# Kernel tuning notes

Measured on AMD Instinct MI355X. Metric: run time of the kernel, lower is better.

## Reference

```python
import math
import jax, jax.numpy as jnp
import numpy as np

DIM = 1536; NH = 12; HD = DIM // NH        # head_dim = 128
F, H, W = 4, 20, 26
S = F * H * W                              # 2080 tokens
BLOCK = 128
SPAD = math.ceil(S / BLOCK) * BLOCK        # 2176
EPS = 1e-6
C = HD // 2
SF, SH, SW = C - 2 * (C // 3), C // 3, C // 3   # 22, 21, 21 rotary bands


def _rope_params(max_len, d, theta=10000.0):
    inv = 1.0 / (theta ** (np.arange(0, d, 2, dtype=np.float64) / d))
    return np.outer(np.arange(max_len), inv)   # [max_len, d//2] angles


def _rope(x, freqs, f, h, w):
    # x: [b, s, n, d] with s == f*h*w; freqs: [1024, d//2] angles
    b, s, n, d = x.shape
    ang = jnp.concatenate([
        jnp.broadcast_to(freqs[:f, :SF][:, None, None, :], (f, h, w, SF)),
        jnp.broadcast_to(freqs[:h, SF:SF + SH][None, :, None, :], (f, h, w, SH)),
        jnp.broadcast_to(freqs[:w, SF + SH:C][None, None, :, :], (f, h, w, SW)),
    ], axis=-1).reshape(s, C)
    cos = jnp.cos(ang)[None, :, None, :]
    sin = jnp.sin(ang)[None, :, None, :]
    xr = x.reshape(b, s, n, C, 2)
    x0, x1 = xr[..., 0], xr[..., 1]          # complex mult (x0+ix1)*(cos+isin)
    out = jnp.stack([x0 * cos - x1 * sin, x0 * sin + x1 * cos], axis=-1)
    return out.reshape(b, s, n, d)


def setup_inputs():
    key = jax.random.key(0)
    ks = jax.random.split(key, 6)
    freqs = jnp.asarray(np.concatenate([
        _rope_params(1024, 2 * SF), _rope_params(1024, 2 * SH), _rope_params(1024, 2 * SW)
    ], axis=1), dtype=jnp.float32)           # [1024, 64]
    lin = lambda k: jax.random.normal(k, (DIM, DIM), jnp.float32) * 0.02
    blk = jnp.arange(SPAD) // BLOCK
    # block-causal (128-token blocks) mask, padding keys (>= S) masked out
    mask = (blk[:, None] >= blk[None, :]) & (jnp.arange(SPAD)[None, :] < S)
    return {
        "x": jax.random.normal(ks[0], (1, S, DIM), jnp.float32),
        "freqs": freqs,
        "wq": lin(ks[1]), "bq": jnp.zeros((DIM,), jnp.float32),
        "wk": lin(ks[2]), "bk": jnp.zeros((DIM,), jnp.float32),
        "wv": lin(ks[3]), "bv": jnp.zeros((DIM,), jnp.float32),
        "wo": lin(ks[4]), "bo": jnp.zeros((DIM,), jnp.float32),
        "gq": jnp.ones((DIM,), jnp.float32),
        "gk": jnp.ones((DIM,), jnp.float32),
        "seq_lens": jnp.array([S], jnp.int32),
        "grid_sizes": jnp.array([[F, H, W]], jnp.int32),
        "mask": mask,
    }


def reference(x, freqs, wq, bq, wk, bk, wv, bv, wo, bo, gq, gk, seq_lens, grid_sizes, mask):
    b, s, _ = x.shape
    n, d = NH, HD
    rms = lambda t, g: (t * jax.lax.rsqrt(jnp.mean(t * t, axis=-1, keepdims=True) + EPS)) * g
    q = rms(x @ wq + bq, gq).reshape(b, s, n, d)
    k = rms(x @ wk + bk, gk).reshape(b, s, n, d)
    v = (x @ wv + bv).reshape(b, s, n, d)
    f, h, w = int(grid_sizes[0, 0]), int(grid_sizes[0, 1]), int(grid_sizes[0, 2])
    sl = int(seq_lens[0])
    if sl > 0 and s == 2 * sl:  # teacher forcing: rope each half independently
        q = jnp.concatenate([_rope(q[:, :sl], freqs, f, h, w), _rope(q[:, sl:], freqs, f, h, w)], axis=1)
        k = jnp.concatenate([_rope(k[:, :sl], freqs, f, h, w), _rope(k[:, sl:], freqs, f, h, w)], axis=1)
    else:
        q = _rope(q, freqs, f, h, w)
        k = _rope(k, freqs, f, h, w)
    pad = SPAD - s
    if pad > 0:
        pz = ((0, 0), (0, pad), (0, 0), (0, 0))
        q, k, v = jnp.pad(q, pz), jnp.pad(k, pz), jnp.pad(v, pz)
    scores = jnp.einsum('bqnd,bknd->bnqk', q, k) / math.sqrt(d)
    scores = jnp.where(mask[None, None], scores, -jnp.inf)
    attn = jax.nn.softmax(scores, axis=-1)
    o = jnp.einsum('bnqk,bknd->bqnd', attn, v)[:, :s].reshape(b, s, n * d)
    return o @ wo + bo
```

## Files before the change

### kernel.cpp

```cpp
#include <hip/hip_runtime.h>

#define DIMM   1536
#define NHEAD  12
#define HD     128
#define SEQ    2080
#define SPADN  2176
#define HWPROD 520
#define SCALE  0.08838834764831845f
#define K2F    0.12751744154f

typedef short short8  __attribute__((ext_vector_type(8)));
typedef float floatx4 __attribute__((ext_vector_type(4)));

__device__ __forceinline__ unsigned short f2bf(float f) {
    union { float f; unsigned u; } v; v.f = f;
    return (unsigned short)((v.u + 0x7fffu + ((v.u >> 16) & 1u)) >> 16);
}
__device__ __forceinline__ float bf2f(unsigned short u) {
    union { unsigned u; float f; } v; v.u = ((unsigned)u) << 16;
    return v.f;
}

__device__ __forceinline__ void gld_lds16(const void* g, void* l) {
    __builtin_amdgcn_global_load_lds(
        (const __attribute__((address_space(1))) unsigned int*)g,
        (__attribute__((address_space(3))) unsigned int*)l, 16, 0, 0);
}

__constant__ int c_base4[34] = {0,1,2,3, 4,6,8,10, 12,15,18,21, 24,28,32,36,
                                40,45,50,55, 60,66,72,78, 84,91,98,105,
                                112,120,128,136, 144, 153};
#define SLOTS_PER_HEAD 153

__global__ void k_prep(const float* __restrict__ x,
                       const float* __restrict__ w0, const float* __restrict__ w1,
                       const float* __restrict__ w2, const float* __restrict__ w3,
                       unsigned short* __restrict__ xb,
                       unsigned short* __restrict__ t0, unsigned short* __restrict__ t1,
                       unsigned short* __restrict__ t2, unsigned short* __restrict__ t3) {
    int z = blockIdx.z;
    if (z == 4) {
        int n4 = SEQ * DIMM / 4;
        int idx = (blockIdx.y * 24 + blockIdx.x) * 256 + threadIdx.x;
#pragma unroll
        for (int i = 0; i < 6; i++) {
            int p = idx + i * 147456;
            if (p < n4) {
                float4 v = ((const float4*)x)[p];
                ushort4 o;
                o.x = f2bf(v.x); o.y = f2bf(v.y); o.z = f2bf(v.z); o.w = f2bf(v.w);
                ((ushort4*)xb)[p] = o;
            }
        }
        return;
    }
    const float* in = (z == 0) ? w0 : (z == 1) ? w1 : (z == 2) ? w2 : w3;
    unsigned short* out = (z == 0) ? t0 : (z == 1) ? t1 : (z == 2) ? t2 : t3;
    __shared__ float tile[64][65];
    int tx = threadIdx.x & 63, ty = threadIdx.x >> 6;
    int r0 = blockIdx.x * 64, c0 = blockIdx.y * 64;
#pragma unroll
    for (int i = 0; i < 16; i++)
        tile[i * 4 + ty][tx] = in[(size_t)(r0 + i * 4 + ty) * DIMM + c0 + tx];
    __syncthreads();
#pragma unroll
    for (int i = 0; i < 16; i++) {
        int cc = i * 4 + ty;
        out[(size_t)(c0 + cc) * DIMM + r0 + tx] = f2bf(tile[tx][cc]);
    }
}

__global__ __launch_bounds__(256, 3) void k_gemm(
    const unsigned short* __restrict__ A,
    const unsigned short* __restrict__ B0, const unsigned short* __restrict__ B1,
    const unsigned short* __restrict__ B2,
    const float* __restrict__ bias0, const float* __restrict__ bias1, const float* __restrict__ bias2,
    unsigned short* __restrict__ Qh, unsigned short* __restrict__ Kh,
    unsigned short* __restrict__ Vt,
    int M, int N, int K) {
    const unsigned short* B = B0; const float* bias = bias0;
    if (blockIdx.z == 1) { B = B1; bias = bias1; }
    if (blockIdx.z == 2) { B = B2; bias = bias2; }

    __shared__ unsigned short As[128 * 64];
    __shared__ unsigned short Bs[128 * 64];

    int tid = threadIdx.x;
    int lane = tid & 63, wv = tid >> 6;
    int quad = lane >> 4, l16 = lane & 15;
    int m0 = blockIdx.y * 128, n0 = blockIdx.x * 128;
    int wm = (wv >> 1) * 64, wn = (wv & 1) * 64;
    int sw = l16 & 7;

    int srow_in_blk = lane >> 3;
    int schunk = lane & 7;
    int gchunk = schunk ^ (srow_in_blk & 7);

    floatx4 acc[4][4];
#pragma unroll
    for (int i = 0; i < 4; i++)
#pragma unroll
        for (int j = 0; j < 4; j++) acc[i][j] = (floatx4){0.f, 0.f, 0.f, 0.f};

    for (int k0 = 0; k0 < K; k0 += 64) {
#pragma unroll
        for (int i = 0; i < 4; i++) {
            int blkrow = (wv * 4 + i) * 8;
            int r = blkrow + srow_in_blk;
            int ra = m0 + r; if (ra > M - 1) ra = M - 1;
            gld_lds16(A + (size_t)ra * K + k0 + gchunk * 8, &As[blkrow * 64]);
            gld_lds16(B + (size_t)(n0 + r) * K + k0 + gchunk * 8, &Bs[blkrow * 64]);
        }
        __syncthreads();
#pragma unroll
        for (int kc = 0; kc < 2; kc++) {
            short8 af[4], bfr[4];
#pragma unroll
            for (int t = 0; t < 4; t++) {
                int ca = ((kc * 4 + quad) ^ sw) << 3;
                af[t]  = *(const short8*)&As[(wm + t * 16 + l16) * 64 + ca];
                bfr[t] = *(const short8*)&Bs[(wn + t * 16 + l16) * 64 + ca];
            }
#pragma unroll
            for (int mi = 0; mi < 4; mi++)
#pragma unroll
                for (int ni = 0; ni < 4; ni++)
                    acc[mi][ni] = __builtin_amdgcn_mfma_f32_16x16x32_bf16(af[mi], bfr[ni], acc[mi][ni], 0, 0, 0);
        }
        __syncthreads();
    }
    if (blockIdx.z == 2) {
#pragma unroll
        for (int mi = 0; mi < 4; mi++) {
            int row0 = m0 + wm + mi * 16 + quad * 4;
            if (row0 < M) {
#pragma unroll
                for (int ni = 0; ni < 4; ni++) {
                    int col = n0 + wn + ni * 16 + l16;
                    float b = bias[col];
                    ushort4 o;
                    o.x = f2bf(acc[mi][ni][0] + b);
                    o.y = f2bf(acc[mi][ni][1] + b);
                    o.z = f2bf(acc[mi][ni][2] + b);
                    o.w = f2bf(acc[mi][ni][3] + b);
                    *(ushort4*)(Vt + (size_t)col * SPADN + row0) = o;
                }
            }
        }
    } else {
        unsigned short* O = (blockIdx.z == 0) ? Qh : Kh;
#pragma unroll
        for (int mi = 0; mi < 4; mi++) {
#pragma unroll
            for (int r = 0; r < 4; r++) {
                int row = m0 + wm + mi * 16 + quad * 4 + r;
                if (row < M) {
#pragma unroll
                    for (int ni = 0; ni < 4; ni++) {
                        int col = n0 + wn + ni * 16 + l16;
                        O[(size_t)row * DIMM + col] = f2bf(acc[mi][ni][r] + bias[col]);
                    }
                }
            }
        }
    }
}

__global__ __launch_bounds__(256, 8) void k_gemm64(
    const unsigned short* __restrict__ A, const unsigned short* __restrict__ B,
    const float* __restrict__ bias, float* __restrict__ C, int M, int N, int K) {
    __shared__ unsigned short As[64 * 64];
    __shared__ unsigned short Bs[64 * 64];
    int tid = threadIdx.x;
    int lane = tid & 63, wv = tid >> 6;
    int quad = lane >> 4, l16 = lane & 15;
    int m0 = blockIdx.y * 64, n0 = blockIdx.x * 64;
    int wm = (wv >> 1) * 32, wn = (wv & 1) * 32;

    int srow = lane >> 3;
    int schunk = lane & 7;

    floatx4 acc[2][2];
#pragma unroll
    for (int i = 0; i < 2; i++)
#pragma unroll
        for (int j = 0; j < 2; j++) acc[i][j] = (floatx4){0.f, 0.f, 0.f, 0.f};

    for (int k0 = 0; k0 < K; k0 += 64) {
#pragma unroll
        for (int i = 0; i < 2; i++) {
            int rb = (i * 4 + wv) * 8;
            int r = rb + srow;
            int g = schunk ^ (r & 7);
            int ra = m0 + r; if (ra > M - 1) ra = M - 1;
            gld_lds16(A + (size_t)ra * K + k0 + g * 8, &As[rb * 64]);
            gld_lds16(B + (size_t)(n0 + r) * K + k0 + g * 8, &Bs[rb * 64]);
        }
        __syncthreads();
#pragma unroll
        for (int kc = 0; kc < 2; kc++) {
            short8 af[2], bfr[2];
#pragma unroll
            for (int t = 0; t < 2; t++) {
                int rowa = wm + t * 16 + l16;
                int rowb = wn + t * 16 + l16;
                int c = kc * 4 + quad;
                af[t]  = *(const short8*)&As[rowa * 64 + ((c ^ (rowa & 7)) << 3)];
                bfr[t] = *(const short8*)&Bs[rowb * 64 + ((c ^ (rowb & 7)) << 3)];
            }
#pragma unroll
            for (int mi = 0; mi < 2; mi++)
#pragma unroll
                for (int ni = 0; ni < 2; ni++)
                    acc[mi][ni] = __builtin_amdgcn_mfma_f32_16x16x32_bf16(af[mi], bfr[ni], acc[mi][ni], 0, 0, 0);
        }
        __syncthreads();
    }
#pragma unroll
    for (int mi = 0; mi < 2; mi++) {
#pragma unroll
        for (int r = 0; r < 4; r++) {
            int row = m0 + wm + mi * 16 + quad * 4 + r;
            if (row < M) {
#pragma unroll
                for (int ni = 0; ni < 2; ni++) {
                    int col = n0 + wn + ni * 16 + l16;
                    C[(size_t)row * N + col] = acc[mi][ni][r] + bias[col];
                }
            }
        }
    }
}

__global__ void k_rmsrope(const unsigned short* __restrict__ Qh, const unsigned short* __restrict__ Kh,
                          const float* __restrict__ gq, const float* __restrict__ gk,
                          const float* __restrict__ freqs,
                          unsigned short* __restrict__ Qa, unsigned short* __restrict__ Ka) {
    __shared__ float redq[4], redk[4];
    int s = blockIdx.x;
    int tid = threadIdx.x;
    int lane = tid & 63, wv = tid >> 6;
    const ushort2* qrow = (const ushort2*)(Qh + (size_t)s * DIMM);
    const ushort2* krow = (const ushort2*)(Kh + (size_t)s * DIMM);
    const float2* g2q = (const float2*)gq;
    const float2* g2k = (const float2*)gk;

    float2 qv[3], kv[3];
    float sq = 0.f, sk = 0.f;
#pragma unroll
    for (int j = 0; j < 3; j++) {
        int p = tid + j * 256;
        ushort2 uq = qrow[p], uk = krow[p];
        qv[j].x = bf2f(uq.x); qv[j].y = bf2f(uq.y);
        kv[j].x = bf2f(uk.x); kv[j].y = bf2f(uk.y);
        sq += qv[j].x * qv[j].x + qv[j].y * qv[j].y;
        sk += kv[j].x * kv[j].x + kv[j].y * kv[j].y;
    }
#pragma unroll
    for (int m = 32; m >= 1; m >>= 1) { sq += __shfl_xor(sq, m); sk += __shfl_xor(sk, m); }
    if (lane == 0) { redq[wv] = sq; redk[wv] = sk; }
    __syncthreads();
    float tq = redq[0] + redq[1] + redq[2] + redq[3];
    float tk = redk[0] + redk[1] + redk[2] + redk[3];
    float scq = rsqrtf(tq * (1.f / DIMM) + 1e-6f);
    float sck = rsqrtf(tk * (1.f / DIMM) + 1e-6f);

    int fi = s / HWPROD;
    int rem = s - fi * HWPROD;
    int hi = rem / 26;
    int wi = rem - hi * 26;
#pragma unroll
    for (int j = 0; j < 3; j++) {
        int p = tid + j * 256;
        int c = p & 63;
        int pos = (c < 22) ? fi : ((c < 43) ? hi : wi);
        float ang = freqs[pos * 64 + c];
        float sn, cs;
        __sincosf(ang, &sn, &cs);
        float2 gqa = g2q[p];
        float q0 = qv[j].x * scq * gqa.x, q1 = qv[j].y * scq * gqa.y;
        ushort2 oq; oq.x = f2bf(q0 * cs - q1 * sn); oq.y = f2bf(q0 * sn + q1 * cs);
        float2 gka = g2k[p];
        float kk0 = kv[j].x * sck * gka.x, kk1 = kv[j].y * sck * gka.y;
        ushort2 ok; ok.x = f2bf(kk0 * cs - kk1 * sn); ok.y = f2bf(kk0 * sn + kk1 * cs);
        int h = p >> 6;
        size_t off = ((size_t)h * SPADN + s) * HD + 2 * c;
        *(ushort2*)(Qa + off) = oq;
        *(ushort2*)(Ka + off) = ok;
    }
}

__global__ __launch_bounds__(256, 3) void k_attn1(const unsigned short* __restrict__ Qa,
                                                  const unsigned short* __restrict__ Ka,
                                                  const unsigned short* __restrict__ Vt,
                                                  unsigned short* __restrict__ Opart,
                                                  float* __restrict__ Lpart,
                                                  unsigned short* __restrict__ Ob) {
    int s = blockIdx.x, h = blockIdx.y;
    int j = 0;
    while (j < 32 && c_base4[j + 1] <= s) j++;
    int z = s - c_base4[j];
    int nkb = (j >> 1) * 2 + 2;
    if (nkb > 33) nkb = 33;
    int nc = (nkb + 3) >> 2;
    int kb0 = z * 4;
    int kb1 = kb0 + 4; if (kb1 > nkb) kb1 = nkb;

    __shared__ unsigned short Ks[64 * 128];
    __shared__ unsigned short Vs[128 * 64];
    __shared__ unsigned short Ps[4][16][72];

    int tid = threadIdx.x;
    int lane = tid & 63, wv = tid >> 6;
    int quad = lane >> 4, l16 = lane & 15;
    int qrow0 = j * 64 + wv * 16;

    short8 qf[4];
#pragma unroll
    for (int kc = 0; kc < 4; kc++)
        qf[kc] = *(const short8*)(Qa + ((size_t)h * SPADN + qrow0 + l16) * HD + kc * 32 + quad * 8);

    short8 ones8;
#pragma unroll
    for (int i = 0; i < 8; i++) ones8[i] = (short)0x3F80;

    floatx4 of[8], of9;
#pragma unroll
    for (int ni = 0; ni < 8; ni++) of[ni] = (floatx4){0.f, 0.f, 0.f, 0.f};
    of9 = (floatx4){0.f, 0.f, 0.f, 0.f};

    int krow = lane >> 4;
    int kslot = lane & 15;
    int vrow = lane >> 3;
    int vslot = lane & 7;

    for (int kb = kb0; kb < kb1; kb++) {
        const unsigned short* kbase = Ka + (((size_t)h * SPADN + kb * 64) * HD);
#pragma unroll
        for (int i = 0; i < 4; i++) {
            int rb = i * 4 + wv;
            int r = rb * 4 + krow;
            int g = (kslot & 8) | ((kslot & 7) ^ (r & 7));
            gld_lds16(kbase + r * 128 + g * 8, &Ks[rb * 512]);
        }
#pragma unroll
        for (int i = 0; i < 4; i++) {
            int rb = i * 4 + wv;
            int r = rb * 8 + vrow;
            int g = vslot ^ (r & 7);
            gld_lds16(Vt + ((size_t)h * HD + r) * SPADN + kb * 64 + g * 8, &Vs[rb * 512]);
        }
        __syncthreads();

        floatx4 sa[4];
#pragma unroll
        for (int ni = 0; ni < 4; ni++) sa[ni] = (floatx4){0.f, 0.f, 0.f, 0.f};
#pragma unroll
        for (int kc = 0; kc < 4; kc++) {
            int c = kc * 4 + quad;
            short8 kf[4];
#pragma unroll
            for (int ni = 0; ni < 4; ni++) {
                int row = ni * 16 + l16;
                int slot = (c & 8) | ((c & 7) ^ (row & 7));
                kf[ni] = *(const short8*)&Ks[row * 128 + slot * 8];
            }
#pragma unroll
            for (int ni = 0; ni < 4; ni++)
                sa[ni] = __builtin_amdgcn_mfma_f32_16x16x32_bf16(qf[kc], kf[ni], sa[ni], 0, 0, 0);
        }

        if (kb != 32) {
#pragma unroll
            for (int r = 0; r < 4; r++) {
#pragma unroll
                for (int ni = 0; ni < 4; ni++) {
                    float p = exp2f(sa[ni][r] * K2F);
                    Ps[wv][quad * 4 + r][ni * 16 + l16] =
                        (unsigned short)(__float_as_uint(p) >> 16);
                }
            }
        } else {
#pragma unroll
            for (int r = 0; r < 4; r++) {
#pragma unroll
                for (int ni = 0; ni < 4; ni++) {
                    bool pad = (kb * 64 + ni * 16 + l16 >= SEQ);
                    float p = pad ? 0.f : exp2f(sa[ni][r] * K2F);
                    Ps[wv][quad * 4 + r][ni * 16 + l16] =
                        (unsigned short)(__float_as_uint(p) >> 16);
                }
            }
        }
#pragma unroll
        for (int kc = 0; kc < 2; kc++) {
            int ko = kc * 32 + quad * 8;
            int c = kc * 4 + quad;
            short8 pf = *(const short8*)&Ps[wv][l16][ko];
#pragma unroll
            for (int ni = 0; ni < 8; ni++) {
                int row = ni * 16 + l16;
                short8 vf = *(const short8*)&Vs[row * 64 + ((c ^ (row & 7)) << 3)];
                of[ni] = __builtin_amdgcn_mfma_f32_16x16x32_bf16(pf, vf, of[ni], 0, 0, 0);
            }
            of9 = __builtin_amdgcn_mfma_f32_16x16x32_bf16(pf, ones8, of9, 0, 0, 0);
        }
        __syncthreads();
    }

    if (nc == 1) {
#pragma unroll
        for (int r = 0; r < 4; r++) {
            float inv = 1.f / of9[r];
            int row = qrow0 + quad * 4 + r;
#pragma unroll
            for (int ni = 0; ni < 8; ni++)
                Ob[(size_t)row * DIMM + h * HD + ni * 16 + l16] = f2bf(of[ni][r] * inv);
        }
    } else {
        int slot = h * SLOTS_PER_HEAD + s;
        unsigned short* Op = Opart + (size_t)slot * 8192;
#pragma unroll
        for (int r = 0; r < 4; r++) {
            int lrow = wv * 16 + quad * 4 + r;
#pragma unroll
            for (int ni = 0; ni < 8; ni++)
                Op[lrow * 128 + ni * 16 + l16] = f2bf(of[ni][r]);
        }
        if (l16 == 0) {
#pragma unroll
            for (int r = 0; r < 4; r++)
                Lpart[slot * 64 + wv * 16 + quad * 4 + r] = of9[r];
        }
    }
}

__global__ void k_attn2(const unsigned short* __restrict__ Opart,
                        const float* __restrict__ Lpart,
                        unsigned short* __restrict__ Ob) {
    int j = blockIdx.x, h = blockIdx.y;
    int nkb = (j >> 1) * 2 + 2; if (nkb > 33) nkb = 33;
    int nc = (nkb + 3) >> 2;
    if (nc == 1) return;
    int base = h * SLOTS_PER_HEAD + c_base4[j];
    int t = threadIdx.x;
    int r = t >> 2;
    int c0 = (t & 3) * 32;
    int row = j * 64 + r;
    if (row >= SEQ) return;

    float acc[32];
#pragma unroll
    for (int q = 0; q < 32; q++) acc[q] = 0.f;
    float L = 0.f;
    for (int c = 0; c < nc; c++) {
        int slot = base + c;
        L += Lpart[slot * 64 + r];
        const ushort4* op = (const ushort4*)(Opart + (size_t)slot * 8192 + r * 128 + c0);
#pragma unroll
        for (int q = 0; q < 8; q++) {
            ushort4 u = op[q];
            acc[q * 4 + 0] += bf2f(u.x); acc[q * 4 + 1] += bf2f(u.y);
            acc[q * 4 + 2] += bf2f(u.z); acc[q * 4 + 3] += bf2f(u.w);
        }
    }
    float inv = 1.f / L;
    unsigned short* ob = Ob + (size_t)row * DIMM + h * HD + c0;
#pragma unroll
    for (int q = 0; q < 8; q++) {
        ushort4 o;
        o.x = f2bf(acc[q * 4 + 0] * inv); o.y = f2bf(acc[q * 4 + 1] * inv);
        o.z = f2bf(acc[q * 4 + 2] * inv); o.w = f2bf(acc[q * 4 + 3] * inv);
        *(ushort4*)(ob + q * 4) = o;
    }
}

extern "C" void kernel_launch(void* const* d_in, const int* in_sizes, int n_in,
                              void* d_out, int out_size, void* d_ws, size_t ws_size,
                              hipStream_t stream) {
    const float* x     = (const float*)d_in[0];
    const float* freqs = (const float*)d_in[1];
    const float* wq    = (const float*)d_in[2];
    const float* bq    = (const float*)d_in[3];
    const float* wk    = (const float*)d_in[4];
    const float* bk    = (const float*)d_in[5];
    const float* wv    = (const float*)d_in[6];
    const float* bv    = (const float*)d_in[7];
    const float* wo    = (const float*)d_in[8];
    const float* bo    = (const float*)d_in[9];
    const float* gq    = (const float*)d_in[10];
    const float* gk    = (const float*)d_in[11];
    float* out = (float*)d_out;

    char* ws = (char*)d_ws;
    size_t off = 0;
    auto alloc = [&](size_t bytes) -> void* {
        void* p = ws + off;
        off += (bytes + 255) & ~(size_t)255;
        return p;
    };
    unsigned short* xb  = (unsigned short*)alloc((size_t)SPADN * DIMM * 2);
    unsigned short* wqT = (unsigned short*)alloc((size_t)DIMM * DIMM * 2);
    unsigned short* wkT = (unsigned short*)alloc((size_t)DIMM * DIMM * 2);
    unsigned short* wvT = (unsigned short*)alloc((size_t)DIMM * DIMM * 2);
    unsigned short* Qh  = (unsigned short*)alloc((size_t)SEQ * DIMM * 2);
    unsigned short* Kh  = (unsigned short*)alloc((size_t)SEQ * DIMM * 2);
    unsigned short* woT = (unsigned short*)alloc((size_t)DIMM * DIMM * 2);
    unsigned short* Qa  = (unsigned short*)alloc((size_t)NHEAD * SPADN * HD * 2);
    unsigned short* Ka  = (unsigned short*)alloc((size_t)NHEAD * SPADN * HD * 2);
    unsigned short* Vt  = (unsigned short*)alloc((size_t)DIMM * SPADN * 2);
    unsigned short* Ob  = (unsigned short*)alloc((size_t)SEQ * DIMM * 2);
    float* Lpart = (float*)alloc((size_t)12 * SLOTS_PER_HEAD * 64 * 4);
    unsigned short* Opart = (unsigned short*)ws;
    (void)ws_size; (void)in_sizes; (void)n_in; (void)out_size;

    k_prep<<<dim3(24, 24, 5), 256, 0, stream>>>(x, wq, wk, wv, wo, xb, wqT, wkT, wvT, woT);
    k_gemm<<<dim3(12, 17, 3), 256, 0, stream>>>(xb, wqT, wkT, wvT, bq, bk, bv,
                                                Qh, Kh, Vt, SEQ, DIMM, DIMM);
    k_rmsrope<<<SEQ, 256, 0, stream>>>(Qh, Kh, gq, gk, freqs, Qa, Ka);
    k_attn1<<<dim3(SLOTS_PER_HEAD, 12), 256, 0, stream>>>(Qa, Ka, Vt, Opart, Lpart, Ob);
    k_attn2<<<dim3(33, 12), 256, 0, stream>>>(Opart, Lpart, Ob);
    k_gemm64<<<dim3(24, 33), 256, 0, stream>>>(Ob, woT, bo, out, SEQ, DIMM, DIMM);
}
```

Before: 240.8 us.

## Transpose weights without LDS, XOR-swizzle P tile, raise attention occupancy

```diff
diff --git a/kernel.cpp b/kernel.cpp
--- a/kernel.cpp
+++ b/kernel.cpp
@@ -38,13 +38,14 @@
                        unsigned short* __restrict__ xb,
                        unsigned short* __restrict__ t0, unsigned short* __restrict__ t1,
                        unsigned short* __restrict__ t2, unsigned short* __restrict__ t3) {
+    int tid = threadIdx.x;
     int z = blockIdx.z;
     if (z == 4) {
         int n4 = SEQ * DIMM / 4;
-        int idx = (blockIdx.y * 24 + blockIdx.x) * 256 + threadIdx.x;
-#pragma unroll
-        for (int i = 0; i < 6; i++) {
-            int p = idx + i * 147456;
+        int idx = (blockIdx.y * 24 + blockIdx.x) * 256 + tid;
+#pragma unroll
+        for (int i = 0; i < 22; i++) {
+            int p = idx + i * 36864;
             if (p < n4) {
                 float4 v = ((const float4*)x)[p];
                 ushort4 o;
@@ -56,17 +57,19 @@
     }
     const float* in = (z == 0) ? w0 : (z == 1) ? w1 : (z == 2) ? w2 : w3;
     unsigned short* out = (z == 0) ? t0 : (z == 1) ? t1 : (z == 2) ? t2 : t3;
-    __shared__ float tile[64][65];
-    int tx = threadIdx.x & 63, ty = threadIdx.x >> 6;
-    int r0 = blockIdx.x * 64, c0 = blockIdx.y * 64;
-#pragma unroll
-    for (int i = 0; i < 16; i++)
-        tile[i * 4 + ty][tx] = in[(size_t)(r0 + i * 4 + ty) * DIMM + c0 + tx];
-    __syncthreads();
+    int n0 = blockIdx.x * 64, k0 = blockIdx.y * 256;
+    int n = n0 + (tid & 63);
+    int ks = tid >> 6;
 #pragma unroll
     for (int i = 0; i < 16; i++) {
-        int cc = i * 4 + ty;
-        out[(size_t)(c0 + cc) * DIMM + r0 + tx] = f2bf(tile[tx][cc]);
+        int k4 = k0 + (ks + i * 4) * 4;
+        float a = in[(size_t)(k4 + 0) * DIMM + n];
+        float b = in[(size_t)(k4 + 1) * DIMM + n];
+        float c = in[(size_t)(k4 + 2) * DIMM + n];
+        float d = in[(size_t)(k4 + 3) * DIMM + n];
+        ushort4 o;
+        o.x = f2bf(a); o.y = f2bf(b); o.z = f2bf(c); o.w = f2bf(d);
+        *(ushort4*)(out + (size_t)n * DIMM + k4) = o;
     }
 }
 
@@ -290,7 +293,7 @@
     }
 }
 
-__global__ __launch_bounds__(256, 3) void k_attn1(const unsigned short* __restrict__ Qa,
+__global__ __launch_bounds__(256, 4) void k_attn1(const unsigned short* __restrict__ Qa,
                                                   const unsigned short* __restrict__ Ka,
                                                   const unsigned short* __restrict__ Vt,
                                                   unsigned short* __restrict__ Opart,
@@ -308,7 +311,7 @@
 
     __shared__ unsigned short Ks[64 * 128];
     __shared__ unsigned short Vs[128 * 64];
-    __shared__ unsigned short Ps[4][16][72];
+    __shared__ unsigned short Ps[4][16][64];
 
     int tid = threadIdx.x;
     int lane = tid & 63, wv = tid >> 6;
@@ -333,6 +336,7 @@
     int kslot = lane & 15;
     int vrow = lane >> 3;
     int vslot = lane & 7;
+    int prow7 = (quad * 4) & 7;
 
     for (int kb = kb0; kb < kb1; kb++) {
         const unsigned short* kbase = Ka + (((size_t)h * SPADN + kb * 64) * HD);
@@ -373,30 +377,35 @@
         if (kb != 32) {
 #pragma unroll
             for (int r = 0; r < 4; r++) {
+                int pr = quad * 4 + r;
+                int rx = (prow7 + r) & 7;
 #pragma unroll
                 for (int ni = 0; ni < 4; ni++) {
                     float p = exp2f(sa[ni][r] * K2F);
-                    Ps[wv][quad * 4 + r][ni * 16 + l16] =
+                    int chunk = ni * 2 + (l16 >> 3);
+                    Ps[wv][pr][((chunk ^ rx) << 3) + (l16 & 7)] =
                         (unsigned short)(__float_as_uint(p) >> 16);
                 }
             }
         } else {
 #pragma unroll
             for (int r = 0; r < 4; r++) {
+                int pr = quad * 4 + r;
+                int rx = (prow7 + r) & 7;
 #pragma unroll
                 for (int ni = 0; ni < 4; ni++) {
                     bool pad = (kb * 64 + ni * 16 + l16 >= SEQ);
                     float p = pad ? 0.f : exp2f(sa[ni][r] * K2F);
-                    Ps[wv][quad * 4 + r][ni * 16 + l16] =
+                    int chunk = ni * 2 + (l16 >> 3);
+                    Ps[wv][pr][((chunk ^ rx) << 3) + (l16 & 7)] =
                         (unsigned short)(__float_as_uint(p) >> 16);
                 }
             }
         }
 #pragma unroll
         for (int kc = 0; kc < 2; kc++) {
-            int ko = kc * 32 + quad * 8;
             int c = kc * 4 + quad;
-            short8 pf = *(const short8*)&Ps[wv][l16][ko];
+            short8 pf = *(const short8*)&Ps[wv][l16][(c ^ (l16 & 7)) << 3];
 #pragma unroll
             for (int ni = 0; ni < 8; ni++) {
                 int row = ni * 16 + l16;
@@ -514,7 +523,7 @@
     unsigned short* Opart = (unsigned short*)ws;
     (void)ws_size; (void)in_sizes; (void)n_in; (void)out_size;
 
-    k_prep<<<dim3(24, 24, 5), 256, 0, stream>>>(x, wq, wk, wv, wo, xb, wqT, wkT, wvT, woT);
+    k_prep<<<dim3(24, 6, 5), 256, 0, stream>>>(x, wq, wk, wv, wo, xb, wqT, wkT, wvT, woT);
     k_gemm<<<dim3(12, 17, 3), 256, 0, stream>>>(xb, wqT, wkT, wvT, bq, bk, bv,
                                                 Qh, Kh, Vt, SEQ, DIMM, DIMM);
     k_rmsrope<<<SEQ, 256, 0, stream>>>(Qh, Kh, gq, gk, freqs, Qa, Ka);
```

After: 260.9 us. +8.4%, slower.
